# Optimization experiments

Hardware: AMD Instinct MI355X
Metric: run time of the kernel (lower is better)

## Reference

```python
import jax, jax.numpy as jnp
import numpy as np

D_MODEL = 2048
N_HEADS = 8
N_KV = 4
HEAD_DIM = 256
WINDOW = 1024
EPS = 1e-6
ROPE_BASE = 10000.0


def _rms_norm(x, w):
    # x: [..., D]; matches torch: x * rsqrt(mean(x^2) + eps) * w
    return x * jax.lax.rsqrt(jnp.mean(x * x, axis=-1, keepdims=True) + EPS) * w


def _rope_cos_sin(pos):
    # pos: [T] ints -> cos/sin: [T, HEAD_DIM] (cat(freqs, freqs) as in source)
    inv_freq = 1.0 / (ROPE_BASE ** (jnp.arange(0, HEAD_DIM, 2, dtype=jnp.float32) / HEAD_DIM))
    freqs = pos.astype(jnp.float32)[:, None] * inv_freq[None, :]  # [T, D/2]
    emb = jnp.concatenate([freqs, freqs], axis=-1)                # [T, D]
    return jnp.cos(emb), jnp.sin(emb)


def _apply_rotary(x, cos, sin):
    # x: [B, H, T, D]; interleaved rotate-half exactly as the torch code
    x1 = x[..., 0::2]
    x2 = x[..., 1::2]
    x_rot = jnp.stack([-x2, x1], axis=-1).reshape(x.shape)
    return x * cos[None, None, :, :] + x_rot * sin[None, None, :, :]


def setup_inputs() -> dict:
    key = jax.random.key(0)
    ks = jax.random.split(key, 8)
    B, T = 1, 4096
    s = 0.02
    return {
        "x": jax.random.normal(ks[0], (B, T, D_MODEL), dtype=jnp.float32),
        "pos": jnp.arange(T, dtype=jnp.int32),
        "Wq": jax.random.normal(ks[1], (N_HEADS * HEAD_DIM, D_MODEL), dtype=jnp.float32) * s,
        "Wk": jax.random.normal(ks[2], (N_KV * HEAD_DIM, D_MODEL), dtype=jnp.float32) * s,
        "Wv": jax.random.normal(ks[3], (N_KV * HEAD_DIM, D_MODEL), dtype=jnp.float32) * s,
        "Wo": jax.random.normal(ks[4], (D_MODEL, N_HEADS * HEAD_DIM), dtype=jnp.float32) * s,
        "q_norm_w": jnp.ones((HEAD_DIM,), dtype=jnp.float32),
        "k_norm_w": jnp.ones((HEAD_DIM,), dtype=jnp.float32),
    }


def reference(x, pos, Wq, Wk, Wv, Wo, q_norm_w, k_norm_w):
    B, T, _ = x.shape
    # projections (torch Linear: y = x @ W.T)
    q = (x @ Wq.T).reshape(B, T, N_HEADS, HEAD_DIM).transpose(0, 2, 1, 3)  # [B,H,T,D]
    k = (x @ Wk.T).reshape(B, T, N_KV, HEAD_DIM).transpose(0, 2, 1, 3)    # [B,Hkv,T,D]
    v = (x @ Wv.T).reshape(B, T, N_KV, HEAD_DIM).transpose(0, 2, 1, 3)
    # per-head RMSNorm
    q = _rms_norm(q, q_norm_w)
    k = _rms_norm(k, k_norm_w)
    # RoPE
    cos, sin = _rope_cos_sin(pos)
    q = _apply_rotary(q, cos, sin)
    k = _apply_rotary(k, cos, sin)
    # GQA repeat: [B,Hkv,T,D] -> [B,H,T,D]
    rep = N_HEADS // N_KV
    k = jnp.repeat(k, rep, axis=1)
    v = jnp.repeat(v, rep, axis=1)
    # full scores + sliding-window causal mask (faithful to source)
    scores = jnp.einsum("bhqd,bhkd->bhqk", q, k) / jnp.sqrt(jnp.float32(HEAD_DIM))
    i = jnp.arange(T)[:, None]
    j = jnp.arange(T)[None, :]
    allowed = (j <= i) & (j >= i - WINDOW + 1)  # [T,T]
    scores = jnp.where(allowed[None, None, :, :], scores, -jnp.inf)
    attn = jax.nn.softmax(scores, axis=-1)
    y = jnp.einsum("bhqk,bhkd->bhqd", attn, v)
    y = y.transpose(0, 2, 1, 3).reshape(B, T, N_HEADS * HEAD_DIM)
    return y @ Wo.T
```

## Files before the change

### kernel.cpp

```cpp
#include <hip/hip_runtime.h>
#include <cstdint>
#include <cmath>

typedef __bf16 bf16x8 __attribute__((ext_vector_type(8)));
typedef float  f32x4  __attribute__((ext_vector_type(4)));

#define DEVI __device__ __forceinline__

#define SEQ 4096
#define NH 8
#define NKV 4
#define HD 256
#define WIN 1024

DEVI void gload16(const void* g, void* l) {
  __builtin_amdgcn_global_load_lds((const __attribute__((address_space(1))) void*)g,
                                   (__attribute__((address_space(3))) void*)l,
                                   16, 0, 0);
}

DEVI bf16x8 ld8f(const float* p) {
  const f32x4 a = *(const f32x4*)p;
  const f32x4 b = *(const f32x4*)(p + 4);
  bf16x8 r;
#pragma unroll
  for (int j = 0; j < 4; ++j) { r[j] = (__bf16)a[j]; r[4 + j] = (__bf16)b[j]; }
  return r;
}

DEVI void st1(float* p, float v)  { *p = v; }
DEVI void st1(__bf16* p, float v) { *p = (__bf16)v; }

__global__ __launch_bounds__(256)
void cvt_all(const float* __restrict__ x,  const float* __restrict__ wq,
             const float* __restrict__ wk, const float* __restrict__ wv,
             const float* __restrict__ wo,
             __bf16* __restrict__ xb, __bf16* __restrict__ wqkvb,
             __bf16* __restrict__ wob) {
  const size_t g = (size_t)blockIdx.x * 256 + threadIdx.x;
  const float* src; __bf16* dst; size_t off;
  if      (g < 1048576) { src = x;  dst = xb;               off = g; }
  else if (g < 1572864) { src = wq; dst = wqkvb;            off = g - 1048576; }
  else if (g < 1835008) { src = wk; dst = wqkvb + 4194304;  off = g - 1572864; }
  else if (g < 2097152) { src = wv; dst = wqkvb + 6291456;  off = g - 1835008; }
  else                  { src = wo; dst = wob;              off = g - 2097152; }
  *(bf16x8*)(dst + off * 8) = ld8f(src + off * 8);
}

template <typename TC>
__global__ __launch_bounds__(256, 2)
void gemm_bt(const __bf16* __restrict__ A, const __bf16* __restrict__ B,
             TC* __restrict__ C, int N, int K) {
  __shared__ __bf16 As[128 * 32];
  __shared__ __bf16 Bs[128 * 32];
  const int tid  = threadIdx.x;
  const int lane = tid & 63;
  const int wave = tid >> 6;
  const int l15  = lane & 15;
  const int l4   = lane >> 4;

  const int lin  = blockIdx.x + gridDim.x * blockIdx.y;
  const int xcd  = lin & 7;
  const int kk   = lin >> 3;
  const int row0 = (xcd * 4 + (kk & 3)) * 128;
  const int col0 = (kk >> 2) * 128;

  const int wm   = (wave >> 1) * 64;
  const int wn   = (wave & 1) * 64;

  f32x4 acc[4][4] = {};
  const int r0 = tid >> 2;
  const int c0 = (tid & 3) * 8;

  for (int k0 = 0; k0 < K; k0 += 32) {
    __syncthreads();
    gload16(A + (size_t)(row0 + r0) * K + k0 + c0,      &As[(wave * 64) * 8]);
    gload16(A + (size_t)(row0 + 64 + r0) * K + k0 + c0, &As[(256 + wave * 64) * 8]);
    gload16(B + (size_t)(col0 + r0) * K + k0 + c0,      &Bs[(wave * 64) * 8]);
    gload16(B + (size_t)(col0 + 64 + r0) * K + k0 + c0, &Bs[(256 + wave * 64) * 8]);
    __syncthreads();
    bf16x8 af[4], bfr[4];
#pragma unroll
    for (int i = 0; i < 4; ++i)
      af[i] = *(const bf16x8*)&As[(wm + i * 16 + l15) * 32 + l4 * 8];
#pragma unroll
    for (int i = 0; i < 4; ++i)
      bfr[i] = *(const bf16x8*)&Bs[(wn + i * 16 + l15) * 32 + l4 * 8];
#pragma unroll
    for (int i = 0; i < 4; ++i)
#pragma unroll
      for (int j = 0; j < 4; ++j)
        acc[i][j] = __builtin_amdgcn_mfma_f32_16x16x32_bf16(af[i], bfr[j], acc[i][j], 0, 0, 0);
  }

#pragma unroll
  for (int i = 0; i < 4; ++i) {
#pragma unroll
    for (int reg = 0; reg < 4; ++reg) {
      const int row = row0 + wm + i * 16 + l4 * 4 + reg;
      TC* crow = C + (size_t)row * N + col0 + wn + l15;
#pragma unroll
      for (int j = 0; j < 4; ++j)
        st1(crow + j * 16, acc[i][j][reg]);
    }
  }
}

__global__ __launch_bounds__(256)
void norm_rope(__bf16* __restrict__ qkv,
               const float* __restrict__ qw, const float* __restrict__ kw,
               const int* __restrict__ pos) {
  const int gw   = blockIdx.x * 4 + (threadIdx.x >> 6);
  const int lane = threadIdx.x & 63;
  __bf16* base; const float* w; int t;
  if (gw < SEQ * NH) {
    t = gw >> 3;
    base = qkv + (size_t)t * 4096 + (gw & 7) * HD;
    w = qw;
  } else {
    const int g = gw - SEQ * NH;
    t = g >> 2;
    base = qkv + (size_t)t * 4096 + 2048 + (g & 3) * HD;
    w = kw;
  }

  const int d0 = lane * 4;
  float v[4]; float ss = 0.f;
#pragma unroll
  for (int j = 0; j < 4; ++j) { v[j] = (float)base[d0 + j]; ss += v[j] * v[j]; }
#pragma unroll
  for (int off = 1; off < 64; off <<= 1) ss += __shfl_xor(ss, off);
  const float rms = rsqrtf(ss * (1.0f / 256.0f) + 1e-6f);
  const float p = (float)pos[t];

  float n[4];
#pragma unroll
  for (int j = 0; j < 4; ++j) n[j] = v[j] * rms * w[d0 + j];

  float outv[4];
#pragma unroll
  for (int e = 0; e < 4; e += 2) {
    const int i0 = d0 + e, i1 = i0 + 1;
    const float f0 = exp2f(-(float)(i0 & 127) * 0.103810253f);
    const float f1 = exp2f(-(float)(i1 & 127) * 0.103810253f);
    float s0, cc0, s1, cc1;
    sincosf(p * f0, &s0, &cc0);
    sincosf(p * f1, &s1, &cc1);
    outv[e]     = n[e] * cc0 - n[e + 1] * s0;
    outv[e + 1] = n[e + 1] * cc1 + n[e] * s1;
  }
#pragma unroll
  for (int j = 0; j < 4; ++j) base[d0 + j] = (__bf16)outv[j];
}

__global__ __launch_bounds__(256)
void transpose_v(const __bf16* __restrict__ qkv, __bf16* __restrict__ Vt) {
  __shared__ __bf16 tile[64][72];
  const int tid = threadIdx.x;
  const int tb  = blockIdx.x * 64;
  const int kvh = blockIdx.y >> 2;
  const int db  = (blockIdx.y & 3) * 64;
#pragma unroll
  for (int i = 0; i < 2; ++i) {
    const int s = i * 256 + tid;
    const int r = s >> 3, c = (s & 7) * 8;
    bf16x8 val = *(const bf16x8*)(qkv + (size_t)(tb + r) * 4096 + 3072 + kvh * HD + db + c);
#pragma unroll
    for (int j = 0; j < 8; ++j) tile[r][c + j] = val[j];
  }
  __syncthreads();
#pragma unroll
  for (int i = 0; i < 2; ++i) {
    const int s = i * 256 + tid;
    const int r = s >> 3, c = (s & 7) * 8;
    bf16x8 outv;
#pragma unroll
    for (int j = 0; j < 8; ++j) outv[j] = tile[c + j][r];
    *(bf16x8*)(Vt + (size_t)(kvh * HD + db + r) * SEQ + tb + c) = outv;
  }
}

__global__ __launch_bounds__(256, 2)
void attn_fwd(const __bf16* __restrict__ qkv, const __bf16* __restrict__ Vt,
              __bf16* __restrict__ Y) {
  __shared__ __bf16 Ks2[8][64][32];
  __shared__ __bf16 Vts2[2][256][32];
  __shared__ __bf16 Ps[4][16][72];
  const int tid  = threadIdx.x;
  const int lane = tid & 63;
  const int wave = tid >> 6;
  const int l15  = lane & 15;
  const int l4   = lane >> 4;
  const int q0   = blockIdx.x * 64;
  const int head = blockIdx.y;
  const int kvh  = head >> 1;
  const int qw   = q0 + wave * 16;

  bf16x8 qf[8];
  const __bf16* qrow = qkv + (size_t)(qw + l15) * 4096 + head * HD;
#pragma unroll
  for (int ks = 0; ks < 8; ++ks) {
    bf16x8 t = *(const bf16x8*)(qrow + ks * 32 + l4 * 8);
#pragma unroll
    for (int j = 0; j < 8; ++j) t[j] = (__bf16)((float)t[j] * 0.0625f);
    qf[ks] = t;
  }

  f32x4 o[16] = {};
  float l_run[4] = {0.f, 0.f, 0.f, 0.f};

  int lo = q0 - (WIN - 1); if (lo < 0) lo = 0;
  const int kt0 = lo >> 6;
  const int kt1 = (q0 + 63) >> 6;

  for (int kt = kt0; kt <= kt1; ++kt) {
    const int kb = kt * 64;
    __syncthreads();
#pragma unroll
    for (int i = 0; i < 8; ++i) {
      const int s = i * 256 + tid;
      gload16(qkv + (size_t)(kb + ((s >> 2) & 63)) * 4096 + 2048 + kvh * HD
                  + (s >> 8) * 32 + (s & 3) * 8,
              (char*)Ks2 + (i * 256 + wave * 64) * 16);
    }
#pragma unroll
    for (int i = 0; i < 8; ++i) {
      const int s = i * 256 + tid;
      gload16(Vt + ((size_t)kvh * HD + ((s >> 2) & 255)) * SEQ + kb
                 + (s >> 10) * 32 + (s & 3) * 8,
              (char*)Vts2 + (i * 256 + wave * 64) * 16);
    }
    __syncthreads();

    f32x4 s_acc[4] = {};
#pragma unroll
    for (int kn = 0; kn < 4; ++kn) {
#pragma unroll
      for (int ks = 0; ks < 8; ++ks) {
        bf16x8 kf = *(const bf16x8*)&Ks2[ks][kn * 16 + l15][l4 * 8];
        s_acc[kn] = __builtin_amdgcn_mfma_f32_16x16x32_bf16(qf[ks], kf, s_acc[kn], 0, 0, 0);
      }
    }

#pragma unroll
    for (int reg = 0; reg < 4; ++reg) {
      const int r  = l4 * 4 + reg;
      const int qg = qw + r;
      float ps = 0.f;
#pragma unroll
      for (int kn = 0; kn < 4; ++kn) {
        const int kg = kb + kn * 16 + l15;
        const bool ok = (kg <= qg) && (kg > qg - WIN);
        const float p = ok ? __expf(fminf(s_acc[kn][reg], 34.f) - 34.f) : 0.f;
        ps += p;
        Ps[wave][r][kn * 16 + l15] = (__bf16)p;
      }
      l_run[reg] += ps;
    }

#pragma unroll
    for (int ks2 = 0; ks2 < 2; ++ks2) {
      bf16x8 pf = *(const bf16x8*)&Ps[wave][l15][ks2 * 32 + l4 * 8];
#pragma unroll
      for (int dn = 0; dn < 16; ++dn) {
        bf16x8 vf = *(const bf16x8*)&Vts2[ks2][dn * 16 + l15][l4 * 8];
        o[dn] = __builtin_amdgcn_mfma_f32_16x16x32_bf16(pf, vf, o[dn], 0, 0, 0);
      }
    }
  }

#pragma unroll
  for (int reg = 0; reg < 4; ++reg) {
#pragma unroll
    for (int off = 1; off < 16; off <<= 1)
      l_run[reg] += __shfl_xor(l_run[reg], off);
    const float inv = 1.0f / l_run[reg];
    const int q = qw + l4 * 4 + reg;
    __bf16* yrow = Y + ((size_t)q * NH + head) * HD + l15;
#pragma unroll
    for (int dn = 0; dn < 16; ++dn)
      yrow[dn * 16] = (__bf16)(o[dn][reg] * inv);
  }
}

extern "C" void kernel_launch(void* const* d_in, const int* in_sizes, int n_in,
                              void* d_out, int out_size, void* d_ws, size_t ws_size,
                              hipStream_t stream) {
  (void)in_sizes; (void)n_in; (void)out_size; (void)ws_size;
  const float* x   = (const float*)d_in[0];
  const int*   pos = (const int*)d_in[1];
  const float* Wq  = (const float*)d_in[2];
  const float* Wk  = (const float*)d_in[3];
  const float* Wv  = (const float*)d_in[4];
  const float* Wo  = (const float*)d_in[5];
  const float* qw  = (const float*)d_in[6];
  const float* kw  = (const float*)d_in[7];
  float* out = (float*)d_out;

  char* ws = (char*)d_ws;
  const size_t MB = 1024 * 1024;
  __bf16* qkv_ws = (__bf16*)(ws);
  __bf16* vt_ws  = (__bf16*)(ws + 32 * MB);
  __bf16* y_ws   = (__bf16*)(ws + 40 * MB);
  __bf16* xb     = (__bf16*)(ws + 56 * MB);
  __bf16* wqkvb  = (__bf16*)(ws + 72 * MB);
  __bf16* wob    = (__bf16*)(ws + 88 * MB);

  const dim3 blk(256);
  cvt_all<<<dim3(10240), blk, 0, stream>>>(x, Wq, Wk, Wv, Wo, xb, wqkvb, wob);
  gemm_bt<__bf16><<<dim3(32, 32), blk, 0, stream>>>(xb, wqkvb, qkv_ws, 4096, 2048);
  norm_rope<<<dim3(12288), blk, 0, stream>>>(qkv_ws, qw, kw, pos);
  transpose_v<<<dim3(64, 16), blk, 0, stream>>>(qkv_ws, vt_ws);
  attn_fwd<<<dim3(64, 8), blk, 0, stream>>>(qkv_ws, vt_ws, y_ws);
  gemm_bt<float><<<dim3(32, 16), blk, 0, stream>>>(y_ws, wob, out, 2048, 2048);
}
```

Baseline: 335.8 us.

## Double-buffer K/V tiles, share KV across GQA heads, fuse norm and V-transpose

The attention kernel now runs 512 threads per block, with the two query heads that share a KV head in the same block. Each K/V tile is loaded once for both heads and prefetched into a second LDS buffer while the current tile is computed, which drops one barrier per iteration. The norm/RoPE and V-transpose kernels are merged into a single launch to remove one launch and its gap. The cost is roughly twice the LDS per block (around 146KB), which caps residency at one block per CU, and half as many attention blocks in the grid.

Result: no change. 338.4 us (+0.8%).

```diff
diff --git a/kernel.cpp b/kernel.cpp
--- a/kernel.cpp
+++ b/kernel.cpp
@@ -107,94 +107,112 @@
 }
 
 __global__ __launch_bounds__(256)
-void norm_rope(__bf16* __restrict__ qkv,
-               const float* __restrict__ qw, const float* __restrict__ kw,
-               const int* __restrict__ pos) {
-  const int gw   = blockIdx.x * 4 + (threadIdx.x >> 6);
-  const int lane = threadIdx.x & 63;
-  __bf16* base; const float* w; int t;
-  if (gw < SEQ * NH) {
-    t = gw >> 3;
-    base = qkv + (size_t)t * 4096 + (gw & 7) * HD;
-    w = qw;
+void norm_rope_tv(__bf16* __restrict__ qkv, __bf16* __restrict__ Vt,
+                  const float* __restrict__ qw, const float* __restrict__ kw,
+                  const int* __restrict__ pos) {
+  if (blockIdx.x < 12288) {
+    const int gw   = blockIdx.x * 4 + (threadIdx.x >> 6);
+    const int lane = threadIdx.x & 63;
+    __bf16* base; const float* w; int t;
+    if (gw < SEQ * NH) {
+      t = gw >> 3;
+      base = qkv + (size_t)t * 4096 + (gw & 7) * HD;
+      w = qw;
+    } else {
+      const int g = gw - SEQ * NH;
+      t = g >> 2;
+      base = qkv + (size_t)t * 4096 + 2048 + (g & 3) * HD;
+      w = kw;
+    }
+
+    const int d0 = lane * 4;
+    float v[4]; float ss = 0.f;
+#pragma unroll
+    for (int j = 0; j < 4; ++j) { v[j] = (float)base[d0 + j]; ss += v[j] * v[j]; }
+#pragma unroll
+    for (int off = 1; off < 64; off <<= 1) ss += __shfl_xor(ss, off);
+    const float rms = rsqrtf(ss * (1.0f / 256.0f) + 1e-6f);
+    const float p = (float)pos[t];
+
+    float n[4];
+#pragma unroll
+    for (int j = 0; j < 4; ++j) n[j] = v[j] * rms * w[d0 + j];
+
+    float outv[4];
+#pragma unroll
+    for (int e = 0; e < 4; e += 2) {
+      const int i0 = d0 + e, i1 = i0 + 1;
+      const float f0 = exp2f(-(float)(i0 & 127) * 0.103810253f);
+      const float f1 = exp2f(-(float)(i1 & 127) * 0.103810253f);
+      float s0, cc0, s1, cc1;
+      sincosf(p * f0, &s0, &cc0);
+      sincosf(p * f1, &s1, &cc1);
+      outv[e]     = n[e] * cc0 - n[e + 1] * s0;
+      outv[e + 1] = n[e + 1] * cc1 + n[e] * s1;
+    }
+#pragma unroll
+    for (int j = 0; j < 4; ++j) base[d0 + j] = (__bf16)outv[j];
   } else {
-    const int g = gw - SEQ * NH;
-    t = g >> 2;
-    base = qkv + (size_t)t * 4096 + 2048 + (g & 3) * HD;
-    w = kw;
-  }
-
-  const int d0 = lane * 4;
-  float v[4]; float ss = 0.f;
-#pragma unroll
-  for (int j = 0; j < 4; ++j) { v[j] = (float)base[d0 + j]; ss += v[j] * v[j]; }
-#pragma unroll
-  for (int off = 1; off < 64; off <<= 1) ss += __shfl_xor(ss, off);
-  const float rms = rsqrtf(ss * (1.0f / 256.0f) + 1e-6f);
-  const float p = (float)pos[t];
-
-  float n[4];
-#pragma unroll
-  for (int j = 0; j < 4; ++j) n[j] = v[j] * rms * w[d0 + j];
-
-  float outv[4];
-#pragma unroll
-  for (int e = 0; e < 4; e += 2) {
-    const int i0 = d0 + e, i1 = i0 + 1;
-    const float f0 = exp2f(-(float)(i0 & 127) * 0.103810253f);
-    const float f1 = exp2f(-(float)(i1 & 127) * 0.103810253f);
-    float s0, cc0, s1, cc1;
-    sincosf(p * f0, &s0, &cc0);
-    sincosf(p * f1, &s1, &cc1);
-    outv[e]     = n[e] * cc0 - n[e + 1] * s0;
-    outv[e + 1] = n[e + 1] * cc1 + n[e] * s1;
-  }
-#pragma unroll
-  for (int j = 0; j < 4; ++j) base[d0 + j] = (__bf16)outv[j];
-}
-
-__global__ __launch_bounds__(256)
-void transpose_v(const __bf16* __restrict__ qkv, __bf16* __restrict__ Vt) {
-  __shared__ __bf16 tile[64][72];
-  const int tid = threadIdx.x;
-  const int tb  = blockIdx.x * 64;
-  const int kvh = blockIdx.y >> 2;
-  const int db  = (blockIdx.y & 3) * 64;
-#pragma unroll
-  for (int i = 0; i < 2; ++i) {
-    const int s = i * 256 + tid;
-    const int r = s >> 3, c = (s & 7) * 8;
-    bf16x8 val = *(const bf16x8*)(qkv + (size_t)(tb + r) * 4096 + 3072 + kvh * HD + db + c);
-#pragma unroll
-    for (int j = 0; j < 8; ++j) tile[r][c + j] = val[j];
-  }
-  __syncthreads();
-#pragma unroll
-  for (int i = 0; i < 2; ++i) {
-    const int s = i * 256 + tid;
-    const int r = s >> 3, c = (s & 7) * 8;
-    bf16x8 outv;
-#pragma unroll
-    for (int j = 0; j < 8; ++j) outv[j] = tile[c + j][r];
-    *(bf16x8*)(Vt + (size_t)(kvh * HD + db + r) * SEQ + tb + c) = outv;
-  }
-}
-
-__global__ __launch_bounds__(256, 2)
+    __shared__ __bf16 tile[64][72];
+    const int b   = blockIdx.x - 12288;
+    const int tid = threadIdx.x;
+    const int tb  = (b & 63) * 64;
+    const int yy  = b >> 6;
+    const int kvh = yy >> 2;
+    const int db  = (yy & 3) * 64;
+#pragma unroll
+    for (int i = 0; i < 2; ++i) {
+      const int s = i * 256 + tid;
+      const int r = s >> 3, c = (s & 7) * 8;
+      bf16x8 val = *(const bf16x8*)(qkv + (size_t)(tb + r) * 4096 + 3072 + kvh * HD + db + c);
+#pragma unroll
+      for (int j = 0; j < 8; ++j) tile[r][c + j] = val[j];
+    }
+    __syncthreads();
+#pragma unroll
+    for (int i = 0; i < 2; ++i) {
+      const int s = i * 256 + tid;
+      const int r = s >> 3, c = (s & 7) * 8;
+      bf16x8 outv;
+#pragma unroll
+      for (int j = 0; j < 8; ++j) outv[j] = tile[c + j][r];
+      *(bf16x8*)(Vt + (size_t)(kvh * HD + db + r) * SEQ + tb + c) = outv;
+    }
+  }
+}
+
+__global__ __launch_bounds__(512, 2)
 void attn_fwd(const __bf16* __restrict__ qkv, const __bf16* __restrict__ Vt,
               __bf16* __restrict__ Y) {
-  __shared__ __bf16 Ks2[8][64][32];
-  __shared__ __bf16 Vts2[2][256][32];
-  __shared__ __bf16 Ps[4][16][72];
+  __shared__ __bf16 Ks2[2][8][64][32];
+  __shared__ __bf16 Vts2[2][2][256][32];
+  __shared__ __bf16 Ps[8][16][72];
   const int tid  = threadIdx.x;
   const int lane = tid & 63;
   const int wave = tid >> 6;
   const int l15  = lane & 15;
   const int l4   = lane >> 4;
   const int q0   = blockIdx.x * 64;
-  const int head = blockIdx.y;
-  const int kvh  = head >> 1;
-  const int qw   = q0 + wave * 16;
+  const int kvh  = blockIdx.y;
+  const int head = kvh * 2 + (wave >> 2);
+  const int qw   = q0 + (wave & 3) * 16;
+
+  auto stage = [&](int kb, int buf) {
+#pragma unroll
+    for (int i = 0; i < 4; ++i) {
+      const int s = i * 512 + tid;
+      gload16(qkv + (size_t)(kb + ((s >> 2) & 63)) * 4096 + 2048 + kvh * HD
+                  + (s >> 8) * 32 + (s & 3) * 8,
+              (char*)Ks2[buf] + (i * 512 + wave * 64) * 16);
+    }
+#pragma unroll
+    for (int i = 0; i < 4; ++i) {
+      const int s = i * 512 + tid;
+      gload16(Vt + ((size_t)kvh * HD + ((s >> 2) & 255)) * SEQ + kb
+                 + (s >> 10) * 32 + (s & 3) * 8,
+              (char*)Vts2[buf] + (i * 512 + wave * 64) * 16);
+    }
+  };
 
   bf16x8 qf[8];
   const __bf16* qrow = qkv + (size_t)(qw + l15) * 4096 + head * HD;
@@ -213,31 +231,20 @@
   const int kt0 = lo >> 6;
   const int kt1 = (q0 + 63) >> 6;
 
+  stage(kt0 * 64, kt0 & 1);
+
   for (int kt = kt0; kt <= kt1; ++kt) {
-    const int kb = kt * 64;
+    const int kb  = kt * 64;
+    const int buf = kt & 1;
     __syncthreads();
-#pragma unroll
-    for (int i = 0; i < 8; ++i) {
-      const int s = i * 256 + tid;
-      gload16(qkv + (size_t)(kb + ((s >> 2) & 63)) * 4096 + 2048 + kvh * HD
-                  + (s >> 8) * 32 + (s & 3) * 8,
-              (char*)Ks2 + (i * 256 + wave * 64) * 16);
-    }
-#pragma unroll
-    for (int i = 0; i < 8; ++i) {
-      const int s = i * 256 + tid;
-      gload16(Vt + ((size_t)kvh * HD + ((s >> 2) & 255)) * SEQ + kb
-                 + (s >> 10) * 32 + (s & 3) * 8,
-              (char*)Vts2 + (i * 256 + wave * 64) * 16);
-    }
-    __syncthreads();
+    if (kt < kt1) stage(kb + 64, buf ^ 1);
 
     f32x4 s_acc[4] = {};
 #pragma unroll
     for (int kn = 0; kn < 4; ++kn) {
 #pragma unroll
       for (int ks = 0; ks < 8; ++ks) {
-        bf16x8 kf = *(const bf16x8*)&Ks2[ks][kn * 16 + l15][l4 * 8];
+        bf16x8 kf = *(const bf16x8*)&Ks2[buf][ks][kn * 16 + l15][l4 * 8];
         s_acc[kn] = __builtin_amdgcn_mfma_f32_16x16x32_bf16(qf[ks], kf, s_acc[kn], 0, 0, 0);
       }
     }
@@ -263,7 +270,7 @@
       bf16x8 pf = *(const bf16x8*)&Ps[wave][l15][ks2 * 32 + l4 * 8];
 #pragma unroll
       for (int dn = 0; dn < 16; ++dn) {
-        bf16x8 vf = *(const bf16x8*)&Vts2[ks2][dn * 16 + l15][l4 * 8];
+        bf16x8 vf = *(const bf16x8*)&Vts2[buf][ks2][dn * 16 + l15][l4 * 8];
         o[dn] = __builtin_amdgcn_mfma_f32_16x16x32_bf16(pf, vf, o[dn], 0, 0, 0);
       }
     }
@@ -306,11 +313,9 @@
   __bf16* wqkvb  = (__bf16*)(ws + 72 * MB);
   __bf16* wob    = (__bf16*)(ws + 88 * MB);
 
-  const dim3 blk(256);
-  cvt_all<<<dim3(10240), blk, 0, stream>>>(x, Wq, Wk, Wv, Wo, xb, wqkvb, wob);
-  gemm_bt<__bf16><<<dim3(32, 32), blk, 0, stream>>>(xb, wqkvb, qkv_ws, 4096, 2048);
-  norm_rope<<<dim3(12288), blk, 0, stream>>>(qkv_ws, qw, kw, pos);
-  transpose_v<<<dim3(64, 16), blk, 0, stream>>>(qkv_ws, vt_ws);
-  attn_fwd<<<dim3(64, 8), blk, 0, stream>>>(qkv_ws, vt_ws, y_ws);
-  gemm_bt<float><<<dim3(32, 16), blk, 0, stream>>>(y_ws, wob, out, 2048, 2048);
-}
+  cvt_all<<<dim3(10240), dim3(256), 0, stream>>>(x, Wq, Wk, Wv, Wo, xb, wqkvb, wob);
+  gemm_bt<__bf16><<<dim3(32, 32), dim3(256), 0, stream>>>(xb, wqkvb, qkv_ws, 4096, 2048);
+  norm_rope_tv<<<dim3(13312), dim3(256), 0, stream>>>(qkv_ws, vt_ws, qw, kw, pos);
+  attn_fwd<<<dim3(64, 4), dim3(512), 0, stream>>>(qkv_ws, vt_ws, y_ws);
+  gemm_bt<float><<<dim3(32, 16), dim3(256), 0, stream>>>(y_ws, wob, out, 2048, 2048);
+}
```
